# Kernel tuning notes

Hardware: AMD Instinct MI355X
Metric: run time of the kernel (lower is better)

## Reference

```python
import jax, jax.numpy as jnp
import numpy as np

B, L, D, H = 2, 2048, 1024, 16
NUM_BUCKETS, MAX_DISTANCE = 32, 128


def _rel_pos_buckets(qlen, klen, num_buckets, max_distance):
    """T5-style bidirectional relative position bucketing. Returns [qlen, klen] int32."""
    ctx = jnp.arange(qlen, dtype=jnp.int32)[:, None]
    mem = jnp.arange(klen, dtype=jnp.int32)[None, :]
    rel = mem - ctx  # memory_position - context_position
    nb = num_buckets // 2
    buckets = (rel > 0).astype(jnp.int32) * nb
    n = jnp.abs(rel)
    max_exact = nb // 2
    is_small = n < max_exact
    nf = jnp.maximum(n.astype(jnp.float32), 1.0)
    large = max_exact + (
        jnp.log(nf / max_exact) / np.float32(np.log(max_distance / max_exact)) * (nb - max_exact)
    ).astype(jnp.int32)
    large = jnp.minimum(large, nb - 1)
    return buckets + jnp.where(is_small, n, large)


def setup_inputs() -> dict:
    key = jax.random.key(0)
    ks = jax.random.split(key, 11)
    s = 0.02
    return {
        "x": jax.random.normal(ks[0], (B, L, D), dtype=jnp.float32),
        "mask": jax.random.randint(ks[1], (B, 1, L, L), 0, 2, dtype=jnp.int32),
        "Wq_w": jax.random.normal(ks[2], (D, D), dtype=jnp.float32) * s,
        "Wq_b": jnp.zeros((D,), dtype=jnp.float32),
        "Wk_w": jax.random.normal(ks[3], (D, D), dtype=jnp.float32) * s,
        "Wk_b": jnp.zeros((D,), dtype=jnp.float32),
        "Wv_w": jax.random.normal(ks[4], (D, D), dtype=jnp.float32) * s,
        "Wv_b": jnp.zeros((D,), dtype=jnp.float32),
        "Wo_w": jax.random.normal(ks[5], (D, D), dtype=jnp.float32) * s,
        "Wo_b": jnp.zeros((D,), dtype=jnp.float32),
        "rel_emb": jax.random.normal(ks[6], (NUM_BUCKETS, H), dtype=jnp.float32) * s,
    }


def reference(x, mask, Wq_w, Wq_b, Wk_w, Wk_b, Wv_w, Wv_b, Wo_w, Wo_b, rel_emb):
    b, l, d = x.shape
    h = H
    dk = d // h
    # torch Linear: y = x @ W.T + b
    Q = (x @ Wq_w.T + Wq_b).reshape(b, l, h, dk)
    K = (x @ Wk_w.T + Wk_b).reshape(b, l, h, dk)
    V = (x @ Wv_w.T + Wv_b).reshape(b, l, h, dk)
    scores = jnp.einsum("bqhd,bkhd->bhqk", Q, K) / jnp.sqrt(jnp.float32(dk))
    buckets = _rel_pos_buckets(l, l, NUM_BUCKETS, MAX_DISTANCE)  # [L, L]
    bias = rel_emb[buckets]  # [L, L, H]
    scores = scores + jnp.transpose(bias, (2, 0, 1))[None]  # [1, H, L, L]
    scores = jnp.where(mask == 0, jnp.float32(-1e9), scores)
    attn = jax.nn.softmax(scores, axis=-1)
    out = jnp.einsum("bhqk,bkhd->bqhd", attn, V).reshape(b, l, d)
    return out @ Wo_w.T + Wo_b
```

## Files before the change

### kernel.cpp

```cpp
#include <hip/hip_runtime.h>
#include <hip/hip_fp16.h>

#define B_ 2
#define L_ 2048
#define D_ 1024
#define H_ 16

typedef __attribute__((ext_vector_type(8))) _Float16 f16x8;
typedef __attribute__((ext_vector_type(4))) _Float16 f16x4;
typedef __attribute__((ext_vector_type(2))) __fp16 fp16x2;
typedef __attribute__((ext_vector_type(4))) float f32x4;

#define LOG2E 1.44269504088896f

__device__ __forceinline__ void gload_lds16(const void* g, void* l) {
  __builtin_amdgcn_global_load_lds(
      (const __attribute__((address_space(1))) unsigned int*)g,
      (__attribute__((address_space(3))) unsigned int*)l, 16, 0, 0);
}

__global__ __launch_bounds__(256) void prep(
    const float* __restrict__ x, const float* __restrict__ Wq,
    const float* __restrict__ Wk, const float* __restrict__ Wv,
    const float* __restrict__ Wo, const int* __restrict__ m,
    const float* __restrict__ rel_emb,
    __half* __restrict__ xh, __half* __restrict__ wqh, __half* __restrict__ wkh,
    __half* __restrict__ wvh, __half* __restrict__ woh,
    unsigned long long* __restrict__ bits, float* __restrict__ tab) {
  const int bid = blockIdx.x;
  if (bid < 8192) {
    int i = bid * 256 + threadIdx.x;
    const float* src;
    __half* dst;
    int j;
    if (i < 1048576) {
      src = x; dst = xh; j = i;
    } else {
      int k = i - 1048576;
      int wsel = k >> 18;
      j = k & 262143;
      src = wsel == 0 ? Wq : (wsel == 1 ? Wk : (wsel == 2 ? Wv : Wo));
      dst = wsel == 0 ? wqh : (wsel == 1 ? wkh : (wsel == 2 ? wvh : woh));
    }
    float4 v = ((const float4*)src)[j];
    __half2* o = (__half2*)(dst + (size_t)j * 4);
    o[0] = __floats2half2_rn(v.x, v.y);
    o[1] = __floats2half2_rn(v.z, v.w);
  } else if (bid < 40960) {
    int wword = (bid - 8192) * 4 + (threadIdx.x >> 6);
    int lane = threadIdx.x & 63;
    int v = m[(size_t)wword * 64 + lane];
    unsigned long long bal = __ballot(v != 0);
    if (lane == 0) bits[wword] = bal;
  } else {
    int i = (bid - 40960) * 256 + threadIdx.x;
    if (i >= H_ * 4095) return;
    int h = i / 4095, idx = i - h * 4095;
    int rel = idx - 2047;
    int n = rel < 0 ? -rel : rel;
    int bkt;
    if (n < 8) {
      bkt = n;
    } else {
      float t = logf((float)n / 8.0f) / 2.772588722239781f * 8.0f;
      int v = 8 + (int)t;
      bkt = v < 15 ? v : 15;
    }
    if (rel > 0) bkt += 16;
    tab[i] = rel_emb[bkt * H_ + h] * LOG2E;
  }
}

template <bool CT>
__device__ __forceinline__ void gemm_tile(const __half* __restrict__ A,
                                          const __half* __restrict__ Bw,
                                          int m0, int n0,
                                          __half* sA, __half* sB,
                                          f32x4 (&acc)[4][4],
                                          int lane, int wm, int wn, int t) {
  for (int k0 = 0; k0 < 1024; k0 += 64) {
    __syncthreads();
#pragma unroll
    for (int it = 0; it < 4; ++it) {
      int c = t + it * 256;
      int row = c >> 3, seg = c & 7;
      gload_lds16(A + ((size_t)(m0 + row) << 10) + k0 + seg * 8, sA + c * 8);
      gload_lds16(Bw + ((size_t)(n0 + row) << 10) + k0 + seg * 8, sB + c * 8);
    }
    __syncthreads();
#pragma unroll
    for (int kk = 0; kk < 2; ++kk) {
      const int off = kk * 32 + (lane >> 4) * 8;
      const int rr = lane & 15;
      f16x8 af[4], bf[4];
#pragma unroll
      for (int i = 0; i < 4; ++i) af[i] = *(const f16x8*)&sA[(wm * 64 + i * 16 + rr) * 64 + off];
#pragma unroll
      for (int i = 0; i < 4; ++i) bf[i] = *(const f16x8*)&sB[(wn * 64 + i * 16 + rr) * 64 + off];
#pragma unroll
      for (int mi = 0; mi < 4; ++mi)
#pragma unroll
        for (int ni = 0; ni < 4; ++ni) {
          if (CT)
            acc[mi][ni] = __builtin_amdgcn_mfma_f32_16x16x32_f16(bf[ni], af[mi], acc[mi][ni], 0, 0, 0);
          else
            acc[mi][ni] = __builtin_amdgcn_mfma_f32_16x16x32_f16(af[mi], bf[ni], acc[mi][ni], 0, 0, 0);
        }
    }
  }
}

__global__ __launch_bounds__(256) void gemm_qkv(
    const __half* __restrict__ xh,
    const __half* __restrict__ Wq, const __half* __restrict__ Wk, const __half* __restrict__ Wv,
    const float* __restrict__ bq, const float* __restrict__ bk, const float* __restrict__ bvv,
    __half* __restrict__ Qh, __half* __restrict__ Kh, __half* __restrict__ Vt) {
  __shared__ __align__(16) __half sA[128 * 64];
  __shared__ __align__(16) __half sB[128 * 64];
  const int lin = blockIdx.x;
  const int xcd = lin & 7, idx = lin >> 3;
  const int m0 = (xcd * 4 + (idx & 3)) * 128;
  const int ng = (idx >> 2) * 128;
  const int widx = ng >> 10;
  const int n0 = ng & 1023;
  const __half* Bw = widx == 0 ? Wq : (widx == 1 ? Wk : Wv);
  const float* bias = widx == 0 ? bq : (widx == 1 ? bk : bvv);
  const int t = threadIdx.x, lane = t & 63, w = t >> 6;
  const int wm = w >> 1, wn = w & 1;
  const int lg = lane >> 4, lr = lane & 15;
  f32x4 acc[4][4] = {};
  if (widx == 2) {
    gemm_tile<false>(xh, Bw, m0, n0, sA, sB, acc, lane, wm, wn, t);
#pragma unroll
    for (int mi = 0; mi < 4; ++mi)
#pragma unroll
      for (int ni = 0; ni < 4; ++ni) {
        int m = m0 + wm * 64 + mi * 16 + lg * 4;
        int n = n0 + wn * 64 + ni * 16 + lr;
        float bvx = bias[n];
        int b = m >> 11, l = m & 2047, hh = n >> 6, dd = n & 63;
        f32x4 a = acc[mi][ni];
        size_t base = ((size_t)((b * 16 + hh) * 64 + dd)) * 2048 + l;
        __half2 p0 = __floats2half2_rn(a.x + bvx, a.y + bvx);
        __half2 p1 = __floats2half2_rn(a.z + bvx, a.w + bvx);
        *(__half2*)(Vt + base) = p0;
        *(__half2*)(Vt + base + 2) = p1;
      }
  } else {
    gemm_tile<true>(xh, Bw, m0, n0, sA, sB, acc, lane, wm, wn, t);
    __half* dst = widx == 0 ? Qh : Kh;
    const float scf = widx == 0 ? 0.125f * LOG2E : 1.0f;
#pragma unroll
    for (int mi = 0; mi < 4; ++mi)
#pragma unroll
      for (int ni = 0; ni < 4; ++ni) {
        int m = m0 + wm * 64 + mi * 16 + lr;
        int n = n0 + wn * 64 + ni * 16 + 4 * lg;
        f32x4 bb = *(const f32x4*)&bias[n];
        int b = m >> 11, l = m & 2047, hh = n >> 6, dd = n & 63;
        f16x4 ov;
#pragma unroll
        for (int r = 0; r < 4; ++r) ov[r] = (_Float16)((acc[mi][ni][r] + bb[r]) * scf);
        *(f16x4*)(dst + (((size_t)(b * 16 + hh)) * 2048 + l) * 64 + dd) = ov;
      }
  }
}

__global__ __launch_bounds__(256) void gemm_out(
    const __half* __restrict__ AO, const __half* __restrict__ Wo,
    const float* __restrict__ bo, float* __restrict__ out) {
  __shared__ __align__(16) __half sA[64 * 64];
  __shared__ __align__(16) __half sB[64 * 64];
  const int lin = blockIdx.x;
  const int xcd = lin & 7, idx = lin >> 3;
  const int m0 = (xcd * 8 + (idx & 7)) * 64;
  const int n0 = (idx >> 3) * 64;
  const int t = threadIdx.x, lane = t & 63, w = t >> 6;
  const int wm = w >> 1, wn = w & 1;
  const int lg = lane >> 4, lr = lane & 15;
  f32x4 acc[2][2] = {};
  for (int k0 = 0; k0 < 1024; k0 += 64) {
    __syncthreads();
#pragma unroll
    for (int it = 0; it < 2; ++it) {
      int c = t + it * 256;
      int row = c >> 3, seg = c & 7;
      gload_lds16(AO + ((size_t)(m0 + row) << 10) + k0 + seg * 8, sA + c * 8);
      gload_lds16(Wo + ((size_t)(n0 + row) << 10) + k0 + seg * 8, sB + c * 8);
    }
    __syncthreads();
#pragma unroll
    for (int kk = 0; kk < 2; ++kk) {
      const int off = kk * 32 + lg * 8;
      f16x8 af[2], bf[2];
#pragma unroll
      for (int i = 0; i < 2; ++i) af[i] = *(const f16x8*)&sA[(wm * 32 + i * 16 + lr) * 64 + off];
#pragma unroll
      for (int i = 0; i < 2; ++i) bf[i] = *(const f16x8*)&sB[(wn * 32 + i * 16 + lr) * 64 + off];
#pragma unroll
      for (int mi = 0; mi < 2; ++mi)
#pragma unroll
        for (int ni = 0; ni < 2; ++ni)
          acc[mi][ni] = __builtin_amdgcn_mfma_f32_16x16x32_f16(bf[ni], af[mi], acc[mi][ni], 0, 0, 0);
    }
  }
#pragma unroll
  for (int mi = 0; mi < 2; ++mi)
#pragma unroll
    for (int ni = 0; ni < 2; ++ni) {
      int mm = m0 + wm * 32 + mi * 16 + lr;
      int nn = n0 + wn * 32 + ni * 16 + 4 * lg;
      f32x4 bb = *(const f32x4*)&bo[nn];
      f32x4 vv;
#pragma unroll
      for (int r = 0; r < 4; ++r) vv[r] = acc[mi][ni][r] + bb[r];
      *(f32x4*)(out + (size_t)mm * 1024 + nn) = vv;
    }
}

__device__ __forceinline__ void stage_kv(const __half* __restrict__ Kb,
                                         const __half* __restrict__ Vb, int kt,
                                         __half* kdst, __half* vdst, int t) {
#pragma unroll
  for (int it = 0; it < 2; ++it) {
    int c = t + it * 256;
    int row = c >> 3, seg = c & 7;
    int gs = (seg ^ row) & 7;
    gload_lds16(Kb + ((size_t)(kt + row) << 6) + gs * 8, kdst + c * 8);
    gload_lds16(Vb + ((size_t)row << 11) + kt + gs * 8, vdst + c * 8);
  }
}

__device__ __forceinline__ void attn_tile(
    const __half* kb, const __half* vb,
    unsigned long long mwv, int diff,
    f16x8 aq0, f16x8 aq1,
    const float* sbias, const __half2* lutm2,
    float c_neg, float c_pos, int lg, int lr,
    f32x4 (&o)[4], f32x4& osum, f16x4 ones) {
  __builtin_amdgcn_s_setprio(1);
  f32x4 s[4] = {};
#pragma unroll
  for (int ct = 0; ct < 4; ++ct) {
    int row = ct * 16 + lr;
    const __half* rb = &kb[row * 64];
    f16x8 kf0 = *(const f16x8*)(rb + ((8 * lg) ^ ((row & 7) << 3)));
    f16x8 kf1 = *(const f16x8*)(rb + ((32 + 8 * lg) ^ ((row & 7) << 3)));
    s[ct] = __builtin_amdgcn_mfma_f32_16x16x32_f16(kf0, aq0, s[ct], 0, 0, 0);
    s[ct] = __builtin_amdgcn_mfma_f32_16x16x32_f16(kf1, aq1, s[ct], 0, 0, 0);
  }
  __builtin_amdgcn_s_setprio(0);

  f16x4 bvA[4], bvB[4];
#pragma unroll
  for (int dt = 0; dt < 4; ++dt) {
    int row = dt * 16 + lr;
    bvA[dt] = *(const f16x4*)&vb[row * 64 + ((4 * lg) ^ ((row & 7) << 3))];
  }

  float tsc = 1.0f;
  if (diff >= 143) {
    tsc = exp2f(c_pos);
  } else if (diff <= -191) {
    tsc = exp2f(c_neg);
  } else {
    const int ibase = diff + 4 * lg - lr + 128;
#pragma unroll
    for (int ct = 0; ct < 4; ++ct)
#pragma unroll
      for (int r = 0; r < 4; ++r) {
        int idx = ibase + 16 * ct + r;
        idx = idx < 0 ? 0 : (idx > 256 ? 256 : idx);
        s[ct][r] += sbias[idx];
      }
  }
  const __half th = __float2half(tsc);
  const __half2 ts2{th, th};

  f16x4 pa[4];
#pragma unroll
  for (int ct = 0; ct < 4; ++ct) {
    unsigned bits = (unsigned)(mwv >> (16 * ct + 4 * lg)) & 15u;
    __half2 m01 = __hmul2(lutm2[bits * 2], ts2), m23 = __hmul2(lutm2[bits * 2 + 1], ts2);
    fp16x2 p01 = __builtin_amdgcn_cvt_pkrtz(exp2f(s[ct][0]), exp2f(s[ct][1]));
    fp16x2 p23 = __builtin_amdgcn_cvt_pkrtz(exp2f(s[ct][2]), exp2f(s[ct][3]));
    f16x4 pc;
    ((__half2*)&pc)[0] = __hmul2(*(__half2*)&p01, m01);
    ((__half2*)&pc)[1] = __hmul2(*(__half2*)&p23, m23);
    pa[ct] = pc;
  }

  __builtin_amdgcn_s_setprio(1);
#pragma unroll
  for (int dt = 0; dt < 4; ++dt) {
    int row = dt * 16 + lr;
    bvB[dt] = *(const f16x4*)&vb[row * 64 + ((16 + 4 * lg) ^ ((row & 7) << 3))];
  }
  osum = __builtin_amdgcn_mfma_f32_16x16x16f16(ones, pa[0], osum, 0, 0, 0);
#pragma unroll
  for (int dt = 0; dt < 4; ++dt)
    o[dt] = __builtin_amdgcn_mfma_f32_16x16x16f16(bvA[dt], pa[0], o[dt], 0, 0, 0);

#pragma unroll
  for (int dt = 0; dt < 4; ++dt) {
    int row = dt * 16 + lr;
    bvA[dt] = *(const f16x4*)&vb[row * 64 + ((32 + 4 * lg) ^ ((row & 7) << 3))];
  }
  osum = __builtin_amdgcn_mfma_f32_16x16x16f16(ones, pa[1], osum, 0, 0, 0);
#pragma unroll
  for (int dt = 0; dt < 4; ++dt)
    o[dt] = __builtin_amdgcn_mfma_f32_16x16x16f16(bvB[dt], pa[1], o[dt], 0, 0, 0);

#pragma unroll
  for (int dt = 0; dt < 4; ++dt) {
    int row = dt * 16 + lr;
    bvB[dt] = *(const f16x4*)&vb[row * 64 + ((48 + 4 * lg) ^ ((row & 7) << 3))];
  }
  osum = __builtin_amdgcn_mfma_f32_16x16x16f16(ones, pa[2], osum, 0, 0, 0);
#pragma unroll
  for (int dt = 0; dt < 4; ++dt)
    o[dt] = __builtin_amdgcn_mfma_f32_16x16x16f16(bvA[dt], pa[2], o[dt], 0, 0, 0);

  osum = __builtin_amdgcn_mfma_f32_16x16x16f16(ones, pa[3], osum, 0, 0, 0);
#pragma unroll
  for (int dt = 0; dt < 4; ++dt)
    o[dt] = __builtin_amdgcn_mfma_f32_16x16x16f16(bvB[dt], pa[3], o[dt], 0, 0, 0);
  __builtin_amdgcn_s_setprio(0);
}

__global__ __attribute__((amdgpu_waves_per_eu(4, 4))) __launch_bounds__(256) void attn(
    const __half* __restrict__ Qh, const __half* __restrict__ Kh,
    const __half* __restrict__ Vt, const unsigned long long* __restrict__ mb64,
    const float* __restrict__ tab, __half* __restrict__ AO) {
  const int id = blockIdx.x;
  const int ii = id >> 3;
  const int bh = (id & 7) * 4 + (ii >> 5);
  const int q0 = (ii & 31) * 64;
  const int b = bh >> 4, h = bh & 15;
  const int t = threadIdx.x, lane = t & 63, w = t >> 6;
  const int lg = lane >> 4, lr = lane & 15;

  __shared__ __align__(16) __half sK[2][64 * 64];
  __shared__ __align__(16) __half sV[2][64 * 64];
  __shared__ float sbias[260];
  __shared__ __align__(8) __half lutm[16][4];

  for (int i = t; i < 257; i += 256) sbias[i] = tab[h * 4095 + 1919 + i];
  if (t < 64) {
    int e = t >> 2, j = t & 3;
    lutm[e][j] = ((e >> j) & 1) ? __half(1.0f) : __half(0.0f);
  }

  const size_t bh2048 = (size_t)bh * 2048;
  const int qrow = q0 + w * 16 + lr;
  const __half* qp = Qh + (bh2048 + qrow) * 64 + lg * 8;
  f16x8 aq0 = *(const f16x8*)qp;
  f16x8 aq1 = *(const f16x8*)(qp + 32);

  const __half* Kb = Kh + bh2048 * 64;
  const __half* Vb = Vt + bh2048 * 64;
  const unsigned long long* mrow = mb64 + ((size_t)(b * 2048 + qrow)) * 32;

  f32x4 o[4] = {};
  f32x4 osum = {};
  const f16x4 ones = {(_Float16)1.f, (_Float16)1.f, (_Float16)1.f, (_Float16)1.f};
  const __half2* lutm2 = (const __half2*)&lutm[0][0];

  unsigned long long mw0 = mrow[0], mw1 = mrow[1];

  stage_kv(Kb, Vb, 0, sK[0], sV[0], t);
  __syncthreads();
  const float c_neg = sbias[0], c_pos = sbias[256];
  const int dbase = -q0 - w * 16;

  for (int k0 = 0; k0 < L_; k0 += 128) {
    stage_kv(Kb, Vb, k0 + 64, sK[1], sV[1], t);
    unsigned long long mwa = mrow[(k0 >> 6) + 2];
    attn_tile(sK[0], sV[0], mw0, k0 + dbase, aq0, aq1, sbias, lutm2,
              c_neg, c_pos, lg, lr, o, osum, ones);
    __syncthreads();

    if (k0 + 128 < L_) stage_kv(Kb, Vb, k0 + 128, sK[0], sV[0], t);
    unsigned long long mwb = mrow[(k0 >> 6) + 3];
    attn_tile(sK[1], sV[1], mw1, k0 + 64 + dbase, aq0, aq1, sbias, lutm2,
              c_neg, c_pos, lg, lr, o, osum, ones);
    __syncthreads();

    mw0 = mwa;
    mw1 = mwb;
  }
  const float rl = 1.0f / osum[0];
  const size_t qbase = ((size_t)(b * L_ + q0 + w * 16 + lr)) * D_ + h * 64;
#pragma unroll
  for (int dt = 0; dt < 4; ++dt) {
    f16x4 ov;
#pragma unroll
    for (int r = 0; r < 4; ++r) ov[r] = (_Float16)(o[dt][r] * rl);
    *(f16x4*)(AO + qbase + dt * 16 + 4 * lg) = ov;
  }
}

extern "C" void kernel_launch(void* const* d_in, const int* in_sizes, int n_in,
                              void* d_out, int out_size, void* d_ws, size_t ws_size,
                              hipStream_t stream) {
  const float* x = (const float*)d_in[0];
  const int* mask = (const int*)d_in[1];
  const float* Wq_w = (const float*)d_in[2];
  const float* Wq_b = (const float*)d_in[3];
  const float* Wk_w = (const float*)d_in[4];
  const float* Wk_b = (const float*)d_in[5];
  const float* Wv_w = (const float*)d_in[6];
  const float* Wv_b = (const float*)d_in[7];
  const float* Wo_w = (const float*)d_in[8];
  const float* Wo_b = (const float*)d_in[9];
  const float* rel_emb = (const float*)d_in[10];
  float* out = (float*)d_out;

  char* ws = (char*)d_ws;
  const size_t MB = 1024 * 1024;
  __half* xh = (__half*)(ws);
  __half* wqh = (__half*)(ws + 8 * MB);
  __half* wkh = (__half*)(ws + 10 * MB);
  __half* wvh = (__half*)(ws + 12 * MB);
  __half* woh = (__half*)(ws + 14 * MB);
  __half* Qh = (__half*)(ws + 16 * MB);
  __half* Kh = (__half*)(ws + 24 * MB);
  __half* Vt = (__half*)(ws + 32 * MB);
  unsigned long long* mb64 = (unsigned long long*)(ws + 40 * MB);
  float* tab = (float*)(ws + 48 * MB);
  __half* AO = xh;

  prep<<<41216, 256, 0, stream>>>(x, Wq_w, Wk_w, Wv_w, Wo_w, mask, rel_emb,
                                  xh, wqh, wkh, wvh, woh, mb64, tab);
  gemm_qkv<<<768, 256, 0, stream>>>(xh, wqh, wkh, wvh, Wq_b, Wk_b, Wv_b, Qh, Kh, Vt);
  attn<<<1024, 256, 0, stream>>>(Qh, Kh, Vt, mb64, tab, AO);
  gemm_out<<<1024, 256, 0, stream>>>(AO, woh, Wo_b, out);
}
```

Measured before the change: 170.6 us.

## Store V transposed in key-blocked layout for contiguous LDS staging and reads

The V projection epilogue now writes V^T in a blocked layout of 8-key groups, each holding 64 dims times 8 keys, so an entire 64-key tile is one contiguous 8KB chunk. Staging then issues contiguous 16-byte global-to-LDS loads, and the PV fragment reads use simple constant offsets instead of XOR-swizzled addresses. This cuts address arithmetic and may reduce strided global access, but LDS bank-conflict behaviour changes because the swizzle is gone. The launch attribute also changes from waves_per_eu(4,4) to launch_bounds(256,4), which may alter register allocation.

```diff
diff --git a/kernel.cpp b/kernel.cpp
--- a/kernel.cpp
+++ b/kernel.cpp
@@ -140,7 +140,7 @@
         float bvx = bias[n];
         int b = m >> 11, l = m & 2047, hh = n >> 6, dd = n & 63;
         f32x4 a = acc[mi][ni];
-        size_t base = ((size_t)((b * 16 + hh) * 64 + dd)) * 2048 + l;
+        size_t base = ((size_t)((b * 16 + hh) * 256 + (l >> 3))) * 512 + dd * 8 + (l & 7);
         __half2 p0 = __floats2half2_rn(a.x + bvx, a.y + bvx);
         __half2 p1 = __floats2half2_rn(a.z + bvx, a.w + bvx);
         *(__half2*)(Vt + base) = p0;
@@ -227,7 +227,7 @@
     int row = c >> 3, seg = c & 7;
     int gs = (seg ^ row) & 7;
     gload_lds16(Kb + ((size_t)(kt + row) << 6) + gs * 8, kdst + c * 8);
-    gload_lds16(Vb + ((size_t)row << 11) + kt + gs * 8, vdst + c * 8);
+    gload_lds16(Vb + ((size_t)((kt >> 3) + (c >> 6)) << 9) + (c & 63) * 8, vdst + c * 8);
   }
 }
 
@@ -251,12 +251,12 @@
   }
   __builtin_amdgcn_s_setprio(0);
 
+  const __half* vbase = vb + ((lg >> 1) * 512 + lr * 8 + (lg & 1) * 4);
+
   f16x4 bvA[4], bvB[4];
 #pragma unroll
-  for (int dt = 0; dt < 4; ++dt) {
-    int row = dt * 16 + lr;
-    bvA[dt] = *(const f16x4*)&vb[row * 64 + ((4 * lg) ^ ((row & 7) << 3))];
-  }
+  for (int dt = 0; dt < 4; ++dt)
+    bvA[dt] = *(const f16x4*)(vbase + dt * 128);
 
   float tsc = 1.0f;
   if (diff >= 143) {
@@ -292,30 +292,24 @@
 
   __builtin_amdgcn_s_setprio(1);
 #pragma unroll
-  for (int dt = 0; dt < 4; ++dt) {
-    int row = dt * 16 + lr;
-    bvB[dt] = *(const f16x4*)&vb[row * 64 + ((16 + 4 * lg) ^ ((row & 7) << 3))];
-  }
+  for (int dt = 0; dt < 4; ++dt)
+    bvB[dt] = *(const f16x4*)(vbase + 1024 + dt * 128);
   osum = __builtin_amdgcn_mfma_f32_16x16x16f16(ones, pa[0], osum, 0, 0, 0);
 #pragma unroll
   for (int dt = 0; dt < 4; ++dt)
     o[dt] = __builtin_amdgcn_mfma_f32_16x16x16f16(bvA[dt], pa[0], o[dt], 0, 0, 0);
 
 #pragma unroll
-  for (int dt = 0; dt < 4; ++dt) {
-    int row = dt * 16 + lr;
-    bvA[dt] = *(const f16x4*)&vb[row * 64 + ((32 + 4 * lg) ^ ((row & 7) << 3))];
-  }
+  for (int dt = 0; dt < 4; ++dt)
+    bvA[dt] = *(const f16x4*)(vbase + 2048 + dt * 128);
   osum = __builtin_amdgcn_mfma_f32_16x16x16f16(ones, pa[1], osum, 0, 0, 0);
 #pragma unroll
   for (int dt = 0; dt < 4; ++dt)
     o[dt] = __builtin_amdgcn_mfma_f32_16x16x16f16(bvB[dt], pa[1], o[dt], 0, 0, 0);
 
 #pragma unroll
-  for (int dt = 0; dt < 4; ++dt) {
-    int row = dt * 16 + lr;
-    bvB[dt] = *(const f16x4*)&vb[row * 64 + ((48 + 4 * lg) ^ ((row & 7) << 3))];
-  }
+  for (int dt = 0; dt < 4; ++dt)
+    bvB[dt] = *(const f16x4*)(vbase + 3072 + dt * 128);
   osum = __builtin_amdgcn_mfma_f32_16x16x16f16(ones, pa[2], osum, 0, 0, 0);
 #pragma unroll
   for (int dt = 0; dt < 4; ++dt)
@@ -328,7 +322,7 @@
   __builtin_amdgcn_s_setprio(0);
 }
 
-__global__ __attribute__((amdgpu_waves_per_eu(4, 4))) __launch_bounds__(256) void attn(
+__global__ __launch_bounds__(256, 4) void attn(
     const __half* __restrict__ Qh, const __half* __restrict__ Kh,
     const __half* __restrict__ Vt, const unsigned long long* __restrict__ mb64,
     const float* __restrict__ tab, __half* __restrict__ AO) {
```

Result: no change. 168.9 us (-1.0%).
